# Optimization experiments

Measured on AMD Instinct MI355X. Metric: run time of the kernel, lower is better.

## Reference

```python
import jax, jax.numpy as jnp
import numpy as np

B, D, E, H, L = 32768, 512, 10, 128, 2  # batch, input_dim, max_charts, expert hidden, latent_dim
RH1, RH2 = 256, 128                      # router hidden sizes
TAU = 3.0


def setup_inputs() -> dict:
    key = jax.random.key(0)
    ks = jax.random.split(key, 16)
    rnd = lambda k, *s: (jax.random.normal(k, s, jnp.float32) * 0.05)
    return {
        "x": jax.random.normal(ks[0], (B, D), jnp.float32),
        "u": jax.random.uniform(ks[1], (B, E), jnp.float32),
        # router params (last layer init ~ N(0, 0.01), bias 0, as in _init_router)
        "rw1": rnd(ks[2], D, RH1), "rb1": jnp.zeros((RH1,), jnp.float32),
        "rw2": rnd(ks[3], RH1, RH2), "rb2": jnp.zeros((RH2,), jnp.float32),
        "rw3": jax.random.normal(ks[4], (RH2, E), jnp.float32) * 0.01,
        "rb3": jnp.zeros((E,), jnp.float32),
        # stacked expert params: all 10 experts batched along leading dim
        "ew1": rnd(ks[5], E, D, H), "eb1": rnd(ks[6], E, H),
        "ew2": rnd(ks[7], E, H, H), "eb2": rnd(ks[8], E, H),
        "ew3": rnd(ks[9], E, H, L), "eb3": rnd(ks[10], E, L),
    }


def reference(x, u, rw1, rb1, rw2, rb2, rw3, rb3, ew1, eb1, ew2, eb2, ew3, eb3):
    # router MLP: D -> 256 -> 128 -> E
    h = jax.nn.relu(x @ rw1 + rb1)
    h = jax.nn.relu(h @ rw2 + rb2)
    logits = h @ rw3 + rb3                                  # [B, E]
    # gumbel_softmax(tau=3.0, hard=False): softmax((logits + gumbel)/tau)
    g = -jnp.log(-jnp.log(jnp.clip(u, 1e-10, 1.0)) + 1e-10)
    weights = jax.nn.softmax((logits + g) / TAU, axis=1)    # [B, E]
    # all 10 experts as batched GEMMs (fuses the python loop over charts)
    h1 = jax.nn.relu(jnp.einsum('bi,eio->beo', x, ew1) + eb1[None])   # [B, E, H]
    h2 = jax.nn.relu(jnp.einsum('beh,eho->beo', h1, ew2) + eb2[None]) # [B, E, H]
    zc = jnp.einsum('beh,ehl->bel', h2, ew3) + eb3[None]              # [B, E, L]
    z = jnp.einsum('be,bel->bl', weights, zc)                         # [B, L]
    chart_outputs = jnp.transpose(zc, (1, 0, 2))                      # [E, B, L]
    return z, weights, chart_outputs
```

## Files before the change

kernel.cpp:

```cpp
#include <hip/hip_runtime.h>
#include <stdint.h>

typedef __bf16 bf16x8 __attribute__((ext_vector_type(8)));
typedef float floatx4 __attribute__((ext_vector_type(4)));
typedef unsigned short ushort_t;

__device__ __forceinline__ ushort_t bf16rne(float f) {
    union { float f; unsigned u; } v; v.f = f;
    return (ushort_t)((v.u + 0x7fffu + ((v.u >> 16) & 1u)) >> 16);
}

__device__ __forceinline__ void gl_lds16(const ushort_t* g, ushort_t* l) {
    __builtin_amdgcn_global_load_lds(
        (const __attribute__((address_space(1))) unsigned int*)g,
        (__attribute__((address_space(3))) unsigned int*)l, 16, 0, 0);
}


#define WAIT_VM_LG_BAR(n) do { asm volatile("s_waitcnt vmcnt(" #n ") lgkmcnt(0)" ::: "memory"); __builtin_amdgcn_s_barrier(); } while (0)
#define WAIT_LG_BAR()     do { asm volatile("s_waitcnt lgkmcnt(0)" ::: "memory"); __builtin_amdgcn_s_barrier(); } while (0)

__global__ void prep(const float* __restrict__ x, ushort_t* __restrict__ x16,
                     const float* __restrict__ ew1, ushort_t* __restrict__ ew1t,
                     const float* __restrict__ ew2, ushort_t* __restrict__ ew2t,
                     const float* __restrict__ rw1, ushort_t* __restrict__ rw1t,
                     const float* __restrict__ rw2, ushort_t* __restrict__ rw2t) {
    __shared__ ushort_t sT[64 * 65];
    int b = blockIdx.x, tid = threadIdx.x;
    if (b < 16384) {
        int i = b * 256 + tid;
        float4 f = ((const float4*)x)[i];
        union { ushort_t s[4]; uint2 v; } pk;
        pk.s[0] = bf16rne(f.x); pk.s[1] = bf16rne(f.y);
        pk.s[2] = bf16rne(f.z); pk.s[3] = bf16rne(f.w);
        ((uint2*)x16)[i] = pk.v;
        return;
    }
    const float* in; ushort_t* outp; int K, N, k0, n0;
    int i = b - 16384;
    if (i < 160) {
        int e = i >> 4, t = i & 15;
        in = ew1 + e * 65536; outp = ew1t + e * 65536;
        K = 512; N = 128; k0 = (t >> 1) * 64; n0 = (t & 1) * 64;
    } else if (i < 200) {
        i -= 160; int e = i >> 2, t = i & 3;
        in = ew2 + e * 16384; outp = ew2t + e * 16384;
        K = 128; N = 128; k0 = (t >> 1) * 64; n0 = (t & 1) * 64;
    } else if (i < 232) {
        i -= 200; in = rw1; outp = rw1t;
        K = 512; N = 256; k0 = (i >> 2) * 64; n0 = (i & 3) * 64;
    } else {
        i -= 232; in = rw2; outp = rw2t;
        K = 256; N = 128; k0 = (i >> 1) * 64; n0 = (i & 1) * 64;
    }
    {
        int c = tid & 63, r0 = tid >> 6;
#pragma unroll
        for (int p = 0; p < 16; ++p) {
            int r = r0 * 16 + p;
            sT[c * 65 + r] = bf16rne(in[(size_t)(k0 + r) * N + n0 + c]);
        }
        __syncthreads();
        int rr = tid & 63, c0 = tid >> 6;
#pragma unroll
        for (int p = 0; p < 16; ++p) {
            int cc = c0 * 16 + p;
            outp[(size_t)(n0 + cc) * K + k0 + rr] = sT[cc * 65 + rr];
        }
    }
}

__global__ __launch_bounds__(256, 2)
void fused_main(const ushort_t* __restrict__ x16,
                const ushort_t* __restrict__ rw1t, const float* __restrict__ rb1,
                const ushort_t* __restrict__ rw2t, const float* __restrict__ rb2,
                const float* __restrict__ rw3, const float* __restrict__ rb3,
                const float* __restrict__ u,
                const ushort_t* __restrict__ ew1t, const ushort_t* __restrict__ ew2t,
                const float* __restrict__ eb1, const float* __restrict__ eb2,
                const float* __restrict__ ew3, const float* __restrict__ eb3,
                float* __restrict__ wts, float* __restrict__ chart) {
    __shared__ alignas(16) ushort_t sU[36864];
    __shared__ float sB1[2][128];
    __shared__ float sB2[2][128];
    __shared__ float sW3e[2][256];
    __shared__ float zbuf[128][2];

    const int tid = threadIdx.x;
    const int id = blockIdx.x;
    const int wave = tid >> 6, lane = tid & 63;
    const int ln15 = lane & 15, q = lane >> 4;
    const int wm = (wave & 1) * 64, wn = (wave >> 1) * 64;
    const int mhalf = wm >> 6, nhalf = wn >> 6;
    const int rl = lane >> 2, cl = lane & 3;
    const int sw = (cl ^ ((rl >> 1) & 3)) * 8;
    const int rg0 = wave * 2, rg1 = rg0 + 1;
    const int fslot = (4 * ln15 + (q ^ ((ln15 >> 1) & 3))) * 8;

    if (id < 256) {
        const int rb = (id & 7) * 32 + (id >> 3);
        sB1[tid >> 7][tid & 127] = rb1[tid];
        if (tid < 128) sB2[0][tid] = rb2[tid];
        else sB2[1][tid - 128] = rb2[tid];
        const ushort_t* xblk = x16 + (size_t)rb * 128 * 512;

        auto stage_rt = [&](int dst, int k0, const ushort_t* w1base) {
            gl_lds16(xblk + (size_t)(rg0 * 16 + rl) * 512 + k0 + sw, &sU[dst + rg0 * 512]);
            gl_lds16(xblk + (size_t)(rg1 * 16 + rl) * 512 + k0 + sw, &sU[dst + rg1 * 512]);
            gl_lds16(w1base + (size_t)(rg0 * 16 + rl) * 512 + k0 + sw, &sU[dst + 4096 + rg0 * 512]);
            gl_lds16(w1base + (size_t)(rg1 * 16 + rl) * 512 + k0 + sw, &sU[dst + 4096 + rg1 * 512]);
        };
        auto stage_rw2 = [&](int reg, int half, int ph) {
#pragma unroll
            for (int r = 0; r < 4; ++r) {
                int s = wave * 4 + r;
                int khl = s >> 3, rg = s & 7;
                int kh = half * 2 + khl;
                gl_lds16(rw2t + (size_t)(rg * 16 + rl) * 256 + ph * 128 + kh * 32 + sw,
                         &sU[reg + s * 512]);
            }
        };

        floatx4 acc2[4][4];
#pragma unroll
        for (int i = 0; i < 4; ++i)
#pragma unroll
            for (int j = 0; j < 4; ++j) acc2[i][j] = (floatx4){0.f, 0.f, 0.f, 0.f};

        auto comp_rg2 = [&](int reg, int half) {
#pragma unroll
            for (int khl = 0; khl < 2; ++khl) {
                int kh = half * 2 + khl;
                bf16x8 a[4], b[4];
#pragma unroll
                for (int t = 0; t < 4; ++t) a[t] = *(const bf16x8*)(&sU[reg + (khl * 8 + mhalf * 4 + t) * 512 + fslot]);
#pragma unroll
                for (int t = 0; t < 4; ++t) b[t] = *(const bf16x8*)(&sU[8192 + kh * 4096 + (nhalf * 4 + t) * 512 + lane * 8]);
                __builtin_amdgcn_s_setprio(1);
#pragma unroll
                for (int i = 0; i < 4; ++i)
#pragma unroll
                    for (int j = 0; j < 4; ++j)
                        acc2[i][j] = __builtin_amdgcn_mfma_f32_16x16x32_bf16(a[i], b[j], acc2[i][j], 0, 0, 0);
                __builtin_amdgcn_s_setprio(0);
            }
        };

        for (int ph = 0; ph < 2; ++ph) {
            const ushort_t* w1base = rw1t + (size_t)ph * 65536;

            floatx4 acc[4][4];
#pragma unroll
            for (int i = 0; i < 4; ++i)
#pragma unroll
                for (int j = 0; j < 4; ++j) acc[i][j] = (floatx4){0.f, 0.f, 0.f, 0.f};

            auto comp_rt = [&](int base) {
                bf16x8 a[4], b[4];
#pragma unroll
                for (int t = 0; t < 4; ++t) a[t] = *(const bf16x8*)(&sU[base + 4096 + (mhalf * 4 + t) * 512 + fslot]);
#pragma unroll
                for (int t = 0; t < 4; ++t) b[t] = *(const bf16x8*)(&sU[base + (nhalf * 4 + t) * 512 + fslot]);
                __builtin_amdgcn_s_setprio(1);
#pragma unroll
                for (int i = 0; i < 4; ++i)
#pragma unroll
                    for (int j = 0; j < 4; ++j)
                        acc[i][j] = __builtin_amdgcn_mfma_f32_16x16x32_bf16(a[i], b[j], acc[i][j], 0, 0, 0);
                __builtin_amdgcn_s_setprio(0);
            };

            stage_rt(0, 0, w1base);
            stage_rt(8192, 32, w1base);
            int cb = 0, sb = 16384;
#pragma unroll 1
            for (int p = 0; p < 16; ++p) {
                if (p < 15) { WAIT_VM_LG_BAR(4); } else { WAIT_VM_LG_BAR(0); }
                if (p < 14) stage_rt(sb, (p + 2) * 32, w1base);
                comp_rt(cb);
                cb = cb == 16384 ? 0 : cb + 8192;
                sb = sb == 16384 ? 0 : sb + 8192;
            }
            WAIT_LG_BAR();

            stage_rw2(0, 0, ph);

#pragma unroll
            for (int i = 0; i < 4; ++i) {
                int hbase = wm + 16 * i;
                int kh = hbase >> 5;
                int qhi = (hbase >> 4) & 1;
                int slotq = 2 * qhi + (q >> 1);
                int h0 = hbase + q * 4;
#pragma unroll
                for (int j = 0; j < 4; ++j) {
                    union { ushort_t s[4]; uint2 v; } pk;
#pragma unroll
                    for (int r = 0; r < 4; ++r)
                        pk.s[r] = bf16rne(fmaxf(acc[i][j][r] + sB1[ph][h0 + r], 0.f));
                    *(uint2*)(&sU[8192 + kh * 4096 + (nhalf * 4 + j) * 512 + slotq * 128 + ln15 * 8 + (q & 1) * 4]) = pk.v;
                }
            }

            WAIT_VM_LG_BAR(0);
            stage_rw2(24576, 1, ph);
            comp_rg2(0, 0);
            WAIT_VM_LG_BAR(0);
            comp_rg2(24576, 1);
            WAIT_LG_BAR();
        }

        float* sw3r = (float*)sU;
        float* lgbuf = (float*)(&sU[2560]);
        for (int i = tid; i < 1280; i += 256) sw3r[i] = rw3[i];
        __syncthreads();

        float lg[4][10];
#pragma unroll
        for (int j = 0; j < 4; ++j)
#pragma unroll
            for (int ee = 0; ee < 10; ++ee) lg[j][ee] = 0.f;
#pragma unroll
        for (int i = 0; i < 4; ++i) {
#pragma unroll
            for (int r = 0; r < 4; ++r) {
                int n = wm + i * 16 + q * 4 + r;
                float bias = n < 128 ? sB2[0][n] : sB2[1][n - 128];
                const float* w3r = &sw3r[n * 10];
#pragma unroll
                for (int j = 0; j < 4; ++j) {
                    float val = fmaxf(acc2[i][j][r] + bias, 0.f);
#pragma unroll
                    for (int ee = 0; ee < 10; ++ee) lg[j][ee] += val * w3r[ee];
                }
            }
        }
#pragma unroll
        for (int j = 0; j < 4; ++j)
#pragma unroll
            for (int ee = 0; ee < 10; ++ee) {
                lg[j][ee] += __shfl_xor(lg[j][ee], 16, 64);
                lg[j][ee] += __shfl_xor(lg[j][ee], 32, 64);
            }
        if (wm == 0 && q == 0) {
#pragma unroll
            for (int j = 0; j < 4; ++j) {
                int row = wn + 16 * j + ln15;
#pragma unroll
                for (int ee = 0; ee < 10; ++ee) lgbuf[row * 10 + ee] = lg[j][ee];
            }
        }
        __syncthreads();
        if (wm == 64 && q == 0) {
#pragma unroll
            for (int j = 0; j < 4; ++j) {
                int row = wn + 16 * j + ln15;
#pragma unroll
                for (int ee = 0; ee < 10; ++ee) lgbuf[row * 10 + ee] += lg[j][ee];
            }
        }
        __syncthreads();
        if (tid < 128) {
            int grow = rb * 128 + tid;
            float v[10], mx = -1e30f;
#pragma unroll
            for (int ee = 0; ee < 10; ++ee) {
                float uu = u[(size_t)grow * 10 + ee];
                uu = fminf(fmaxf(uu, 1e-10f), 1.0f);
                float g = -logf(-logf(uu) + 1e-10f);
                v[ee] = (lgbuf[tid * 10 + ee] + rb3[ee] + g) * (1.0f / 3.0f);
                mx = fmaxf(mx, v[ee]);
            }
            float s = 0.f;
#pragma unroll
            for (int ee = 0; ee < 10; ++ee) { v[ee] = expf(v[ee] - mx); s += v[ee]; }
            float inv = 1.0f / s;
#pragma unroll
            for (int ee = 0; ee < 10; ++ee) wts[(size_t)grow * 10 + ee] = v[ee] * inv;
        }
    } else {
        const int eid = id - 256;
        const int xcd = eid & 7, local = eid >> 3;
        const int pr = local % 5;
        const int rb = xcd * 32 + local / 5;
        const int e0 = pr * 2;

        if (tid < 128) {
            sB1[0][tid] = eb1[e0 * 128 + tid];
            sB2[0][tid] = eb2[e0 * 128 + tid];
        } else {
            sB1[1][tid - 128] = eb1[(e0 + 1) * 128 + (tid - 128)];
            sB2[1][tid - 128] = eb2[(e0 + 1) * 128 + (tid - 128)];
        }
        sW3e[0][tid] = ew3[e0 * 256 + tid];
        sW3e[1][tid] = ew3[(e0 + 1) * 256 + tid];

        const ushort_t* xblk = x16 + (size_t)rb * 128 * 512;
        const ushort_t* w1a = ew1t + (size_t)e0 * 65536;
        const ushort_t* w1b = w1a + 65536;

        floatx4 accA[4][4], accB[4][4];
#pragma unroll
        for (int i = 0; i < 4; ++i)
#pragma unroll
            for (int j = 0; j < 4; ++j) {
                accA[i][j] = (floatx4){0.f, 0.f, 0.f, 0.f};
                accB[i][j] = (floatx4){0.f, 0.f, 0.f, 0.f};
            }

        auto stage_g1 = [&](int dst, int k0) {
            gl_lds16(xblk + (size_t)(rg0 * 16 + rl) * 512 + k0 + sw, &sU[dst + rg0 * 512]);
            gl_lds16(xblk + (size_t)(rg1 * 16 + rl) * 512 + k0 + sw, &sU[dst + rg1 * 512]);
            gl_lds16(w1a + (size_t)(rg0 * 16 + rl) * 512 + k0 + sw, &sU[dst + 4096 + rg0 * 512]);
            gl_lds16(w1a + (size_t)(rg1 * 16 + rl) * 512 + k0 + sw, &sU[dst + 4096 + rg1 * 512]);
            gl_lds16(w1b + (size_t)(rg0 * 16 + rl) * 512 + k0 + sw, &sU[dst + 8192 + rg0 * 512]);
            gl_lds16(w1b + (size_t)(rg1 * 16 + rl) * 512 + k0 + sw, &sU[dst + 8192 + rg1 * 512]);
        };
        auto comp_g1 = [&](int base) {
            bf16x8 a0[4], a1[4], b[4];
#pragma unroll
            for (int t = 0; t < 4; ++t) b[t] = *(const bf16x8*)(&sU[base + (nhalf * 4 + t) * 512 + fslot]);
#pragma unroll
            for (int t = 0; t < 4; ++t) a0[t] = *(const bf16x8*)(&sU[base + 4096 + (mhalf * 4 + t) * 512 + fslot]);
#pragma unroll
            for (int t = 0; t < 4; ++t) a1[t] = *(const bf16x8*)(&sU[base + 8192 + (mhalf * 4 + t) * 512 + fslot]);
            __builtin_amdgcn_s_setprio(1);
#pragma unroll
            for (int i = 0; i < 4; ++i)
#pragma unroll
                for (int j = 0; j < 4; ++j) {
                    accA[i][j] = __builtin_amdgcn_mfma_f32_16x16x32_bf16(a0[i], b[j], accA[i][j], 0, 0, 0);
                    accB[i][j] = __builtin_amdgcn_mfma_f32_16x16x32_bf16(a1[i], b[j], accB[i][j], 0, 0, 0);
                }
            __builtin_amdgcn_s_setprio(0);
        };
        auto stage_w2 = [&](const ushort_t* w2, int reg, int half) {
#pragma unroll
            for (int r = 0; r < 4; ++r) {
                int s = wave * 4 + r;
                int khl = s >> 3, rg = s & 7;
                int kh = half * 2 + khl;
                gl_lds16(w2 + (size_t)(rg * 16 + rl) * 128 + kh * 32 + sw, &sU[reg + s * 512]);
            }
        };
        auto comp_g2 = [&](int reg, int half, floatx4 (&acc2)[4][4]) {
#pragma unroll
            for (int khl = 0; khl < 2; ++khl) {
                int kh = half * 2 + khl;
                bf16x8 a[4], b[4];
#pragma unroll
                for (int t = 0; t < 4; ++t) a[t] = *(const bf16x8*)(&sU[reg + (khl * 8 + mhalf * 4 + t) * 512 + fslot]);
#pragma unroll
                for (int t = 0; t < 4; ++t) b[t] = *(const bf16x8*)(&sU[8192 + kh * 4096 + (nhalf * 4 + t) * 512 + lane * 8]);
                __builtin_amdgcn_s_setprio(1);
#pragma unroll
                for (int i = 0; i < 4; ++i)
#pragma unroll
                    for (int j = 0; j < 4; ++j)
                        acc2[i][j] = __builtin_amdgcn_mfma_f32_16x16x32_bf16(a[i], b[j], acc2[i][j], 0, 0, 0);
                __builtin_amdgcn_s_setprio(0);
            }
        };

        stage_g1(0, 0);
        stage_g1(12288, 32);
        int cb = 0, sb = 24576;
#pragma unroll 1
        for (int p = 0; p < 16; ++p) {
            if (p < 15) { WAIT_VM_LG_BAR(6); } else { WAIT_VM_LG_BAR(0); }
            if (p < 14) stage_g1(sb, (p + 2) * 32);
            comp_g1(cb);
            cb = cb == 24576 ? 0 : cb + 12288;
            sb = sb == 24576 ? 0 : sb + 12288;
        }
        WAIT_LG_BAR();

        stage_w2(ew2t + (size_t)e0 * 16384, 0, 0);

#pragma unroll
        for (int ex = 0; ex < 2; ++ex) {
            const int e = e0 + ex;
            const ushort_t* w2 = ew2t + (size_t)e * 16384;

#pragma unroll
            for (int i = 0; i < 4; ++i) {
                int hbase = wm + 16 * i;
                int kh = hbase >> 5;
                int qhi = (hbase >> 4) & 1;
                int slotq = 2 * qhi + (q >> 1);
                int h0 = hbase + q * 4;
#pragma unroll
                for (int j = 0; j < 4; ++j) {
                    union { ushort_t s[4]; uint2 v; } pk;
#pragma unroll
                    for (int r = 0; r < 4; ++r) {
                        float av = ex == 0 ? accA[i][j][r] : accB[i][j][r];
                        pk.s[r] = bf16rne(fmaxf(av + sB1[ex][h0 + r], 0.f));
                    }
                    *(uint2*)(&sU[8192 + kh * 4096 + (nhalf * 4 + j) * 512 + slotq * 128 + ln15 * 8 + (q & 1) * 4]) = pk.v;
                }
            }

            floatx4 acc2[4][4];
#pragma unroll
            for (int i = 0; i < 4; ++i)
#pragma unroll
                for (int j = 0; j < 4; ++j) acc2[i][j] = (floatx4){0.f, 0.f, 0.f, 0.f};

            WAIT_VM_LG_BAR(0);
            stage_w2(w2, 24576, 1);
            comp_g2(0, 0, acc2);
            WAIT_VM_LG_BAR(0);
            if (ex == 0) stage_w2(ew2t + (size_t)(e0 + 1) * 16384, 0, 0);
            comp_g2(24576, 1, acc2);

            float zc0[4] = {0.f, 0.f, 0.f, 0.f}, zc1[4] = {0.f, 0.f, 0.f, 0.f};
#pragma unroll
            for (int i = 0; i < 4; ++i) {
                int o0 = wm + i * 16 + q * 4;
#pragma unroll
                for (int r = 0; r < 4; ++r) {
                    int o = o0 + r;
                    float w3a = sW3e[ex][2 * o], w3b = sW3e[ex][2 * o + 1];
                    float bias = sB2[ex][o];
#pragma unroll
                    for (int j = 0; j < 4; ++j) {
                        float val = fmaxf(acc2[i][j][r] + bias, 0.f);
                        zc0[j] += val * w3a;
                        zc1[j] += val * w3b;
                    }
                }
            }
#pragma unroll
            for (int j = 0; j < 4; ++j) {
                zc0[j] += __shfl_xor(zc0[j], 16, 64);
                zc0[j] += __shfl_xor(zc0[j], 32, 64);
                zc1[j] += __shfl_xor(zc1[j], 16, 64);
                zc1[j] += __shfl_xor(zc1[j], 32, 64);
            }
            if (wm == 0 && q == 0) {
#pragma unroll
                for (int j = 0; j < 4; ++j) {
                    int row = wn + j * 16 + ln15;
                    zbuf[row][0] = zc0[j];
                    zbuf[row][1] = zc1[j];
                }
            }
            __syncthreads();
            if (wm == 64 && q == 0) {
#pragma unroll
                for (int j = 0; j < 4; ++j) {
                    int row = wn + j * 16 + ln15;
                    zbuf[row][0] += zc0[j];
                    zbuf[row][1] += zc1[j];
                }
            }
            __syncthreads();
            {
                int row = tid >> 1, l = tid & 1;
                int grow = rb * 128 + row;
                chart[(size_t)e * 65536 + (size_t)grow * 2 + l] = zbuf[row][l] + eb3[e * 2 + l];
            }
        }
    }
}

__global__ void z_final(const float* __restrict__ w, const float* __restrict__ chart,
                        float* __restrict__ z) {
    __shared__ float swt[2560];
    int b0 = blockIdx.x * 256;
    for (int i = threadIdx.x; i < 2560; i += 256) swt[i] = w[(size_t)b0 * 10 + i];
    __syncthreads();
    int row = b0 + threadIdx.x;
    float z0 = 0.f, z1 = 0.f;
#pragma unroll
    for (int e = 0; e < 10; ++e) {
        float we = swt[threadIdx.x * 10 + e];
        float2 c = *(const float2*)(&chart[(size_t)e * 65536 + (size_t)row * 2]);
        z0 += we * c.x;
        z1 += we * c.y;
    }
    float2 o; o.x = z0; o.y = z1;
    *(float2*)(&z[(size_t)row * 2]) = o;
}

extern "C" void kernel_launch(void* const* d_in, const int* in_sizes, int n_in,
                              void* d_out, int out_size, void* d_ws, size_t ws_size,
                              hipStream_t stream) {
    const float* x = (const float*)d_in[0];
    const float* u = (const float*)d_in[1];
    const float* rw1 = (const float*)d_in[2];
    const float* rb1 = (const float*)d_in[3];
    const float* rw2 = (const float*)d_in[4];
    const float* rb2 = (const float*)d_in[5];
    const float* rw3 = (const float*)d_in[6];
    const float* rb3 = (const float*)d_in[7];
    const float* ew1 = (const float*)d_in[8];
    const float* eb1 = (const float*)d_in[9];
    const float* ew2 = (const float*)d_in[10];
    const float* eb2 = (const float*)d_in[11];
    const float* ew3 = (const float*)d_in[12];
    const float* eb3 = (const float*)d_in[13];
    float* out = (float*)d_out;
    float* z = out;
    float* wts = out + 65536;
    float* chart = out + 393216;

    ushort_t* x16  = (ushort_t*)d_ws;
    ushort_t* ew1t = x16 + 16777216;
    ushort_t* ew2t = ew1t + 655360;
    ushort_t* rw1t = ew2t + 163840;
    ushort_t* rw2t = rw1t + 131072;

    prep<<<16624, 256, 0, stream>>>(x, x16, ew1, ew1t, ew2, ew2t, rw1, rw1t, rw2, rw2t);

    fused_main<<<1536, 256, 0, stream>>>(x16, rw1t, rb1, rw2t, rb2, rw3, rb3, u,
                                         ew1t, ew2t, eb1, eb2, ew3, eb3,
                                         wts, chart);

    z_final<<<128, 256, 0, stream>>>(wts, chart, z);
}
```

Baseline: 207.4 us.

## Load GEMM operands directly from global into registers, bypassing LDS staging

Replaces the LDS-staged, barrier-synchronized double-buffered pipelines for the first and second GEMMs with per-wave direct global-to-register fragment loads, ping-ponged in registers and gated by vmcnt waits. Shared memory shrinks to only the hidden-activation buffer, which removes most barriers and LDS traffic and may improve occupancy. In exchange, each wave re-fetches overlapping x and weight tiles from global/L2 instead of sharing them through LDS, and register pressure rises.

Result: slower. 291.8 us (+40.7%).

```diff
diff --git a/kernel.cpp b/kernel.cpp
--- a/kernel.cpp
+++ b/kernel.cpp
@@ -10,15 +10,9 @@
     return (ushort_t)((v.u + 0x7fffu + ((v.u >> 16) & 1u)) >> 16);
 }
 
-__device__ __forceinline__ void gl_lds16(const ushort_t* g, ushort_t* l) {
-    __builtin_amdgcn_global_load_lds(
-        (const __attribute__((address_space(1))) unsigned int*)g,
-        (__attribute__((address_space(3))) unsigned int*)l, 16, 0, 0);
-}
-
-
-#define WAIT_VM_LG_BAR(n) do { asm volatile("s_waitcnt vmcnt(" #n ") lgkmcnt(0)" ::: "memory"); __builtin_amdgcn_s_barrier(); } while (0)
-#define WAIT_LG_BAR()     do { asm volatile("s_waitcnt lgkmcnt(0)" ::: "memory"); __builtin_amdgcn_s_barrier(); } while (0)
+
+#define WAIT_VM(n)    asm volatile("s_waitcnt vmcnt(" #n ")" ::: "memory")
+#define WAIT_LG_BAR() do { asm volatile("s_waitcnt lgkmcnt(0)" ::: "memory"); __builtin_amdgcn_s_barrier(); } while (0)
 
 __global__ void prep(const float* __restrict__ x, ushort_t* __restrict__ x16,
                      const float* __restrict__ ew1, ushort_t* __restrict__ ew1t,
@@ -80,7 +74,7 @@
                 const float* __restrict__ eb1, const float* __restrict__ eb2,
                 const float* __restrict__ ew3, const float* __restrict__ eb3,
                 float* __restrict__ wts, float* __restrict__ chart) {
-    __shared__ alignas(16) ushort_t sU[36864];
+    __shared__ alignas(16) ushort_t sU[16384];
     __shared__ float sB1[2][128];
     __shared__ float sB2[2][128];
     __shared__ float sW3e[2][256];
@@ -91,35 +85,21 @@
     const int wave = tid >> 6, lane = tid & 63;
     const int ln15 = lane & 15, q = lane >> 4;
     const int wm = (wave & 1) * 64, wn = (wave >> 1) * 64;
-    const int mhalf = wm >> 6, nhalf = wn >> 6;
-    const int rl = lane >> 2, cl = lane & 3;
-    const int sw = (cl ^ ((rl >> 1) & 3)) * 8;
-    const int rg0 = wave * 2, rg1 = rg0 + 1;
-    const int fslot = (4 * ln15 + (q ^ ((ln15 >> 1) & 3))) * 8;
+    const int nhalf = wn >> 6;
 
     if (id < 256) {
         const int rb = (id & 7) * 32 + (id >> 3);
         sB1[tid >> 7][tid & 127] = rb1[tid];
         if (tid < 128) sB2[0][tid] = rb2[tid];
         else sB2[1][tid - 128] = rb2[tid];
+        WAIT_VM(0);
+        __syncthreads();
+
         const ushort_t* xblk = x16 + (size_t)rb * 128 * 512;
-
-        auto stage_rt = [&](int dst, int k0, const ushort_t* w1base) {
-            gl_lds16(xblk + (size_t)(rg0 * 16 + rl) * 512 + k0 + sw, &sU[dst + rg0 * 512]);
-            gl_lds16(xblk + (size_t)(rg1 * 16 + rl) * 512 + k0 + sw, &sU[dst + rg1 * 512]);
-            gl_lds16(w1base + (size_t)(rg0 * 16 + rl) * 512 + k0 + sw, &sU[dst + 4096 + rg0 * 512]);
-            gl_lds16(w1base + (size_t)(rg1 * 16 + rl) * 512 + k0 + sw, &sU[dst + 4096 + rg1 * 512]);
-        };
-        auto stage_rw2 = [&](int reg, int half, int ph) {
-#pragma unroll
-            for (int r = 0; r < 4; ++r) {
-                int s = wave * 4 + r;
-                int khl = s >> 3, rg = s & 7;
-                int kh = half * 2 + khl;
-                gl_lds16(rw2t + (size_t)(rg * 16 + rl) * 256 + ph * 128 + kh * 32 + sw,
-                         &sU[reg + s * 512]);
-            }
-        };
+        const ushort_t* xr[4];
+#pragma unroll
+        for (int t = 0; t < 4; ++t)
+            xr[t] = xblk + (size_t)(wn + t * 16 + ln15) * 512 + q * 8;
 
         floatx4 acc2[4][4];
 #pragma unroll
@@ -127,15 +107,59 @@
 #pragma unroll
             for (int j = 0; j < 4; ++j) acc2[i][j] = (floatx4){0.f, 0.f, 0.f, 0.f};
 
-        auto comp_rg2 = [&](int reg, int half) {
-#pragma unroll
-            for (int khl = 0; khl < 2; ++khl) {
-                int kh = half * 2 + khl;
-                bf16x8 a[4], b[4];
-#pragma unroll
-                for (int t = 0; t < 4; ++t) a[t] = *(const bf16x8*)(&sU[reg + (khl * 8 + mhalf * 4 + t) * 512 + fslot]);
-#pragma unroll
-                for (int t = 0; t < 4; ++t) b[t] = *(const bf16x8*)(&sU[8192 + kh * 4096 + (nhalf * 4 + t) * 512 + lane * 8]);
+        for (int ph = 0; ph < 2; ++ph) {
+            const ushort_t* w1r[4];
+#pragma unroll
+            for (int t = 0; t < 4; ++t)
+                w1r[t] = rw1t + (size_t)ph * 65536 + (size_t)(wm + t * 16 + ln15) * 512 + q * 8;
+
+            floatx4 acc[4][4];
+#pragma unroll
+            for (int i = 0; i < 4; ++i)
+#pragma unroll
+                for (int j = 0; j < 4; ++j) acc[i][j] = (floatx4){0.f, 0.f, 0.f, 0.f};
+
+            bf16x8 sxA[4], saA[4], sxB[4], saB[4];
+            auto load1 = [&](bf16x8 (&sx)[4], bf16x8 (&sa)[4], int k0) {
+#pragma unroll
+                for (int t = 0; t < 4; ++t) sx[t] = *(const bf16x8*)(xr[t] + k0);
+#pragma unroll
+                for (int t = 0; t < 4; ++t) sa[t] = *(const bf16x8*)(w1r[t] + k0);
+            };
+            auto comp1 = [&](bf16x8 (&sx)[4], bf16x8 (&sa)[4]) {
+                __builtin_amdgcn_s_setprio(1);
+#pragma unroll
+                for (int i = 0; i < 4; ++i)
+#pragma unroll
+                    for (int j = 0; j < 4; ++j)
+                        acc[i][j] = __builtin_amdgcn_mfma_f32_16x16x32_bf16(sa[i], sx[j], acc[i][j], 0, 0, 0);
+                __builtin_amdgcn_s_setprio(0);
+            };
+
+            load1(sxA, saA, 0);
+#pragma unroll 1
+            for (int p = 0; p < 16; p += 2) {
+                load1(sxB, saB, (p + 1) * 32);
+                WAIT_VM(8);
+                comp1(sxA, saA);
+                if (p < 14) { load1(sxA, saA, (p + 2) * 32); WAIT_VM(8); }
+                else        { WAIT_VM(0); }
+                comp1(sxB, saB);
+            }
+
+            const ushort_t* w2r[4];
+#pragma unroll
+            for (int t = 0; t < 4; ++t)
+                w2r[t] = rw2t + (size_t)(wm + t * 16 + ln15) * 256 + ph * 128 + q * 8;
+            bf16x8 w2A[4], w2B[4];
+            auto loadW2 = [&](bf16x8 (&s)[4], int kh) {
+#pragma unroll
+                for (int t = 0; t < 4; ++t) s[t] = *(const bf16x8*)(w2r[t] + kh * 32);
+            };
+            auto comp2 = [&](bf16x8 (&a)[4], int kh) {
+                bf16x8 b[4];
+#pragma unroll
+                for (int t = 0; t < 4; ++t) b[t] = *(const bf16x8*)(&sU[kh * 4096 + (nhalf * 4 + t) * 512 + lane * 8]);
                 __builtin_amdgcn_s_setprio(1);
 #pragma unroll
                 for (int i = 0; i < 4; ++i)
@@ -143,48 +167,9 @@
                     for (int j = 0; j < 4; ++j)
                         acc2[i][j] = __builtin_amdgcn_mfma_f32_16x16x32_bf16(a[i], b[j], acc2[i][j], 0, 0, 0);
                 __builtin_amdgcn_s_setprio(0);
-            }
-        };
-
-        for (int ph = 0; ph < 2; ++ph) {
-            const ushort_t* w1base = rw1t + (size_t)ph * 65536;
-
-            floatx4 acc[4][4];
-#pragma unroll
-            for (int i = 0; i < 4; ++i)
-#pragma unroll
-                for (int j = 0; j < 4; ++j) acc[i][j] = (floatx4){0.f, 0.f, 0.f, 0.f};
-
-            auto comp_rt = [&](int base) {
-                bf16x8 a[4], b[4];
-#pragma unroll
-                for (int t = 0; t < 4; ++t) a[t] = *(const bf16x8*)(&sU[base + 4096 + (mhalf * 4 + t) * 512 + fslot]);
-#pragma unroll
-                for (int t = 0; t < 4; ++t) b[t] = *(const bf16x8*)(&sU[base + (nhalf * 4 + t) * 512 + fslot]);
-                __builtin_amdgcn_s_setprio(1);
-#pragma unroll
-                for (int i = 0; i < 4; ++i)
-#pragma unroll
-                    for (int j = 0; j < 4; ++j)
-                        acc[i][j] = __builtin_amdgcn_mfma_f32_16x16x32_bf16(a[i], b[j], acc[i][j], 0, 0, 0);
-                __builtin_amdgcn_s_setprio(0);
-            };
-
-            stage_rt(0, 0, w1base);
-            stage_rt(8192, 32, w1base);
-            int cb = 0, sb = 16384;
-#pragma unroll 1
-            for (int p = 0; p < 16; ++p) {
-                if (p < 15) { WAIT_VM_LG_BAR(4); } else { WAIT_VM_LG_BAR(0); }
-                if (p < 14) stage_rt(sb, (p + 2) * 32, w1base);
-                comp_rt(cb);
-                cb = cb == 16384 ? 0 : cb + 8192;
-                sb = sb == 16384 ? 0 : sb + 8192;
-            }
-            WAIT_LG_BAR();
-
-            stage_rw2(0, 0, ph);
-
+            };
+
+            loadW2(w2A, 0);
 #pragma unroll
             for (int i = 0; i < 4; ++i) {
                 int hbase = wm + 16 * i;
@@ -198,15 +183,14 @@
 #pragma unroll
                     for (int r = 0; r < 4; ++r)
                         pk.s[r] = bf16rne(fmaxf(acc[i][j][r] + sB1[ph][h0 + r], 0.f));
-                    *(uint2*)(&sU[8192 + kh * 4096 + (nhalf * 4 + j) * 512 + slotq * 128 + ln15 * 8 + (q & 1) * 4]) = pk.v;
-                }
-            }
-
-            WAIT_VM_LG_BAR(0);
-            stage_rw2(24576, 1, ph);
-            comp_rg2(0, 0);
-            WAIT_VM_LG_BAR(0);
-            comp_rg2(24576, 1);
+                    *(uint2*)(&sU[kh * 4096 + (nhalf * 4 + j) * 512 + slotq * 128 + ln15 * 8 + (q & 1) * 4]) = pk.v;
+                }
+            }
+            WAIT_LG_BAR();
+            loadW2(w2B, 1); WAIT_VM(4); comp2(w2A, 0);
+            loadW2(w2A, 2); WAIT_VM(4); comp2(w2B, 1);
+            loadW2(w2B, 3); WAIT_VM(4); comp2(w2A, 2);
+                            WAIT_VM(0); comp2(w2B, 3);
             WAIT_LG_BAR();
         }
 
@@ -294,10 +278,18 @@
         }
         sW3e[0][tid] = ew3[e0 * 256 + tid];
         sW3e[1][tid] = ew3[(e0 + 1) * 256 + tid];
+        WAIT_VM(0);
+        __syncthreads();
 
         const ushort_t* xblk = x16 + (size_t)rb * 128 * 512;
         const ushort_t* w1a = ew1t + (size_t)e0 * 65536;
-        const ushort_t* w1b = w1a + 65536;
+
+        const ushort_t* xr[4]; const ushort_t* ar[4];
+#pragma unroll
+        for (int t = 0; t < 4; ++t) {
+            xr[t] = xblk + (size_t)(wn + t * 16 + ln15) * 512 + q * 8;
+            ar[t] = w1a + (size_t)(wm + t * 16 + ln15) * 512 + q * 8;
+        }
 
         floatx4 accA[4][4], accB[4][4];
 #pragma unroll
@@ -308,50 +300,62 @@
                 accB[i][j] = (floatx4){0.f, 0.f, 0.f, 0.f};
             }
 
-        auto stage_g1 = [&](int dst, int k0) {
-            gl_lds16(xblk + (size_t)(rg0 * 16 + rl) * 512 + k0 + sw, &sU[dst + rg0 * 512]);
-            gl_lds16(xblk + (size_t)(rg1 * 16 + rl) * 512 + k0 + sw, &sU[dst + rg1 * 512]);
-            gl_lds16(w1a + (size_t)(rg0 * 16 + rl) * 512 + k0 + sw, &sU[dst + 4096 + rg0 * 512]);
-            gl_lds16(w1a + (size_t)(rg1 * 16 + rl) * 512 + k0 + sw, &sU[dst + 4096 + rg1 * 512]);
-            gl_lds16(w1b + (size_t)(rg0 * 16 + rl) * 512 + k0 + sw, &sU[dst + 8192 + rg0 * 512]);
-            gl_lds16(w1b + (size_t)(rg1 * 16 + rl) * 512 + k0 + sw, &sU[dst + 8192 + rg1 * 512]);
+        bf16x8 sxA[4], saA[4], sbA[4], sxB[4], saB[4], sbB[4];
+        auto load1 = [&](bf16x8 (&sx)[4], bf16x8 (&sa)[4], bf16x8 (&sb)[4], int k0) {
+#pragma unroll
+            for (int t = 0; t < 4; ++t) sx[t] = *(const bf16x8*)(xr[t] + k0);
+#pragma unroll
+            for (int t = 0; t < 4; ++t) sa[t] = *(const bf16x8*)(ar[t] + k0);
+#pragma unroll
+            for (int t = 0; t < 4; ++t) sb[t] = *(const bf16x8*)(ar[t] + 65536 + k0);
         };
-        auto comp_g1 = [&](int base) {
-            bf16x8 a0[4], a1[4], b[4];
-#pragma unroll
-            for (int t = 0; t < 4; ++t) b[t] = *(const bf16x8*)(&sU[base + (nhalf * 4 + t) * 512 + fslot]);
-#pragma unroll
-            for (int t = 0; t < 4; ++t) a0[t] = *(const bf16x8*)(&sU[base + 4096 + (mhalf * 4 + t) * 512 + fslot]);
-#pragma unroll
-            for (int t = 0; t < 4; ++t) a1[t] = *(const bf16x8*)(&sU[base + 8192 + (mhalf * 4 + t) * 512 + fslot]);
+        auto comp1 = [&](bf16x8 (&sx)[4], bf16x8 (&sa)[4], bf16x8 (&sb)[4]) {
             __builtin_amdgcn_s_setprio(1);
 #pragma unroll
             for (int i = 0; i < 4; ++i)
 #pragma unroll
                 for (int j = 0; j < 4; ++j) {
-                    accA[i][j] = __builtin_amdgcn_mfma_f32_16x16x32_bf16(a0[i], b[j], accA[i][j], 0, 0, 0);
-                    accB[i][j] = __builtin_amdgcn_mfma_f32_16x16x32_bf16(a1[i], b[j], accB[i][j], 0, 0, 0);
+                    accA[i][j] = __builtin_amdgcn_mfma_f32_16x16x32_bf16(sa[i], sx[j], accA[i][j], 0, 0, 0);
+                    accB[i][j] = __builtin_amdgcn_mfma_f32_16x16x32_bf16(sb[i], sx[j], accB[i][j], 0, 0, 0);
                 }
             __builtin_amdgcn_s_setprio(0);
         };
-        auto stage_w2 = [&](const ushort_t* w2, int reg, int half) {
-#pragma unroll
-            for (int r = 0; r < 4; ++r) {
-                int s = wave * 4 + r;
-                int khl = s >> 3, rg = s & 7;
-                int kh = half * 2 + khl;
-                gl_lds16(w2 + (size_t)(rg * 16 + rl) * 128 + kh * 32 + sw, &sU[reg + s * 512]);
-            }
-        };
-        auto comp_g2 = [&](int reg, int half, floatx4 (&acc2)[4][4]) {
-#pragma unroll
-            for (int khl = 0; khl < 2; ++khl) {
-                int kh = half * 2 + khl;
-                bf16x8 a[4], b[4];
-#pragma unroll
-                for (int t = 0; t < 4; ++t) a[t] = *(const bf16x8*)(&sU[reg + (khl * 8 + mhalf * 4 + t) * 512 + fslot]);
-#pragma unroll
-                for (int t = 0; t < 4; ++t) b[t] = *(const bf16x8*)(&sU[8192 + kh * 4096 + (nhalf * 4 + t) * 512 + lane * 8]);
+
+        load1(sxA, saA, sbA, 0);
+#pragma unroll 1
+        for (int p = 0; p < 16; p += 2) {
+            load1(sxB, saB, sbB, (p + 1) * 32);
+            WAIT_VM(12);
+            comp1(sxA, saA, sbA);
+            if (p < 14) { load1(sxA, saA, sbA, (p + 2) * 32); WAIT_VM(12); }
+            else        { WAIT_VM(0); }
+            comp1(sxB, saB, sbB);
+        }
+
+#pragma unroll
+        for (int ex = 0; ex < 2; ++ex) {
+            const int e = e0 + ex;
+            const ushort_t* w2 = ew2t + (size_t)e * 16384;
+            const ushort_t* w2r[4];
+#pragma unroll
+            for (int t = 0; t < 4; ++t)
+                w2r[t] = w2 + (size_t)(wm + t * 16 + ln15) * 128 + q * 8;
+            bf16x8 w2A[4], w2B[4];
+            auto loadW2 = [&](bf16x8 (&s)[4], int kh) {
+#pragma unroll
+                for (int t = 0; t < 4; ++t) s[t] = *(const bf16x8*)(w2r[t] + kh * 32);
+            };
+
+            floatx4 acc2[4][4];
+#pragma unroll
+            for (int i = 0; i < 4; ++i)
+#pragma unroll
+                for (int j = 0; j < 4; ++j) acc2[i][j] = (floatx4){0.f, 0.f, 0.f, 0.f};
+
+            auto comp2 = [&](bf16x8 (&a)[4], int kh) {
+                bf16x8 b[4];
+#pragma unroll
+                for (int t = 0; t < 4; ++t) b[t] = *(const bf16x8*)(&sU[kh * 4096 + (nhalf * 4 + t) * 512 + lane * 8]);
                 __builtin_amdgcn_s_setprio(1);
 #pragma unroll
                 for (int i = 0; i < 4; ++i)
@@ -359,29 +363,9 @@
                     for (int j = 0; j < 4; ++j)
                         acc2[i][j] = __builtin_amdgcn_mfma_f32_16x16x32_bf16(a[i], b[j], acc2[i][j], 0, 0, 0);
                 __builtin_amdgcn_s_setprio(0);
-            }
-        };
-
-        stage_g1(0, 0);
-        stage_g1(12288, 32);
-        int cb = 0, sb = 24576;
-#pragma unroll 1
-        for (int p = 0; p < 16; ++p) {
-            if (p < 15) { WAIT_VM_LG_BAR(6); } else { WAIT_VM_LG_BAR(0); }
-            if (p < 14) stage_g1(sb, (p + 2) * 32);
-            comp_g1(cb);
-            cb = cb == 24576 ? 0 : cb + 12288;
-            sb = sb == 24576 ? 0 : sb + 12288;
-        }
-        WAIT_LG_BAR();
-
-        stage_w2(ew2t + (size_t)e0 * 16384, 0, 0);
-
-#pragma unroll
-        for (int ex = 0; ex < 2; ++ex) {
-            const int e = e0 + ex;
-            const ushort_t* w2 = ew2t + (size_t)e * 16384;
-
+            };
+
+            loadW2(w2A, 0);
 #pragma unroll
             for (int i = 0; i < 4; ++i) {
                 int hbase = wm + 16 * i;
@@ -397,22 +381,14 @@
                         float av = ex == 0 ? accA[i][j][r] : accB[i][j][r];
                         pk.s[r] = bf16rne(fmaxf(av + sB1[ex][h0 + r], 0.f));
                     }
-                    *(uint2*)(&sU[8192 + kh * 4096 + (nhalf * 4 + j) * 512 + slotq * 128 + ln15 * 8 + (q & 1) * 4]) = pk.v;
-                }
-            }
-
-            floatx4 acc2[4][4];
-#pragma unroll
-            for (int i = 0; i < 4; ++i)
-#pragma unroll
-                for (int j = 0; j < 4; ++j) acc2[i][j] = (floatx4){0.f, 0.f, 0.f, 0.f};
-
-            WAIT_VM_LG_BAR(0);
-            stage_w2(w2, 24576, 1);
-            comp_g2(0, 0, acc2);
-            WAIT_VM_LG_BAR(0);
-            if (ex == 0) stage_w2(ew2t + (size_t)(e0 + 1) * 16384, 0, 0);
-            comp_g2(24576, 1, acc2);
+                    *(uint2*)(&sU[kh * 4096 + (nhalf * 4 + j) * 512 + slotq * 128 + ln15 * 8 + (q & 1) * 4]) = pk.v;
+                }
+            }
+            WAIT_LG_BAR();
+            loadW2(w2B, 1); WAIT_VM(4); comp2(w2A, 0);
+            loadW2(w2A, 2); WAIT_VM(4); comp2(w2B, 1);
+            loadW2(w2B, 3); WAIT_VM(4); comp2(w2A, 2);
+                            WAIT_VM(0); comp2(w2B, 3);
 
             float zc0[4] = {0.f, 0.f, 0.f, 0.f}, zc1[4] = {0.f, 0.f, 0.f, 0.f};
 #pragma unroll
```
